# Kernel tuning notes

Measured on AMD Instinct MI355X. Metric: run time of the kernel, lower is better.

## Reference

```python
import jax, jax.numpy as jnp
import numpy as np

N_PARTS = 4
HIDDEN = 256
NUM_FREQS = 10
IN_DIM = 3
EMB_DIM = IN_DIM * (1 + 2 * NUM_FREQS)  # 63
PART_DIM = HIDDEN // N_PARTS


def _embed(x):
    freqs = 2.0 ** jnp.arange(NUM_FREQS, dtype=x.dtype)        # [F]
    xf = x[..., None, :] * freqs[:, None]                      # [..., F, 3]
    enc = jnp.stack([jnp.sin(xf), jnp.cos(xf)], axis=-2)       # [..., F, 2, 3]
    enc = enc.reshape(x.shape[:-1] + (NUM_FREQS * 2 * IN_DIM,))
    return jnp.concatenate([x, enc], axis=-1)                  # [..., 63]


def _masks():
    # contiguous 0/1 per-part neuron masks over the HIDDEN axis (ClassMaskCreator)
    m = np.zeros((N_PARTS, HIDDEN), dtype=np.float32)
    for p in range(N_PARTS):
        s = p * PART_DIM
        e = HIDDEN if p == N_PARTS - 1 else s + PART_DIM
        m[p, s:e] = 1.0
    return jnp.asarray(m)


def setup_inputs() -> dict:
    key = jax.random.key(0)
    ks = jax.random.split(key, 8)
    B, N = 1, 131072

    def lin(k, fan_in, fan_out):
        return jax.random.normal(k, (fan_in, fan_out), jnp.float32) / np.float32(np.sqrt(fan_in))

    return {
        "coords": jax.random.normal(ks[0], (B, N, IN_DIM), jnp.float32),
        "W0": lin(ks[1], EMB_DIM, HIDDEN), "b0": jnp.zeros((HIDDEN,), jnp.float32),
        "W1": lin(ks[2], HIDDEN, HIDDEN), "b1": jnp.zeros((HIDDEN,), jnp.float32),
        "W2": lin(ks[3], HIDDEN, HIDDEN), "b2": jnp.zeros((HIDDEN,), jnp.float32),
        "Wocc": lin(ks[4], HIDDEN, 1), "bocc": jnp.zeros((1,), jnp.float32),
        "Wc": jax.random.normal(ks[5], (N_PARTS, HIDDEN), jnp.float32) / np.float32(np.sqrt(HIDDEN)),
        "bc": jnp.zeros((N_PARTS,), jnp.float32),
    }


def reference(coords, W0, b0, W1, b1, W2, b2, Wocc, bocc, Wc, bc):
    masks = _masks()                                  # [P, H]
    x = _embed(coords) @ W0 + b0                      # [B, N, H]  (no activation after layer 0, per source)

    # occupancy trunk: relu(L1) -> relu(L2) -> occ head
    x_occ = jax.nn.relu(x @ W1 + b1)
    x_occ = jax.nn.relu(x_occ @ W2 + b2)
    occ = x_occ @ Wocc + bocc                         # [B, N, 1]

    # part branches. Loop iteration i=0 masks x; i=1 indexes temporal_part_output[1*part_id],
    # i.e. the i=0 outputs. The i=1 outputs (h2) are dead w.r.t. all returned values because
    # part_features[part_id] for part_id in 0..P-1 selects the first P (i=0) entries.
    h1 = [jax.nn.relu((x * masks[p]) @ W1 + b1) for p in range(N_PARTS)]  # [B, N, H] each

    # class heads: class_heads[p](h1[p] * mask_p).squeeze(0), concatenated on last dim
    cls = [jnp.squeeze((h1[p] * masks[p]) @ Wc[p][:, None] + bc[p], axis=0)
           for p in range(N_PARTS)]                   # [N, 1] each (B == 1)
    part_class = jnp.concatenate(cls, axis=-1)        # [N, P]

    return occ, part_class
```

## Files before the change

kernel.cpp:

```cpp
#include <hip/hip_runtime.h>


#define NPTS 131072
#define M_PB 128
#define AST 256

typedef _Float16 half8   __attribute__((ext_vector_type(8)));
typedef _Float16 half4_t __attribute__((ext_vector_type(4)));
typedef __fp16   fp16x2  __attribute__((ext_vector_type(2)));
typedef float    float4_t __attribute__((ext_vector_type(4)));

__global__ void prep(const float* __restrict__ W0, const float* __restrict__ W1,
                     const float* __restrict__ W2, _Float16* __restrict__ ws) {
  int id = blockIdx.x * 256 + threadIdx.x;
  _Float16 v;
  if (id < 16384) {
    int e = id, j = e & 7, l = (e >> 3) & 63, tn = (e >> 9) & 3, kb = (e >> 11) & 1, s = e >> 12;
    int k = kb * 32 + (l >> 4) * 8 + j, n = s * 64 + tn * 16 + (l & 15);
    v = (k < 63) ? (_Float16)W0[k * 256 + n] : (_Float16)0.f;
  } else if (id < 81920) {
    int e = id - 16384, j = e & 7, l = (e >> 3) & 63, tn = (e >> 9) & 3, kb = (e >> 11) & 7, s = e >> 14;
    int k = kb * 32 + (l >> 4) * 8 + j, n = s * 64 + tn * 16 + (l & 15);
    v = (_Float16)W1[k * 256 + n];
  } else {
    int e = id - 81920, j = e & 7, l = (e >> 3) & 63, tn = (e >> 9) & 3, kb = (e >> 11) & 7, s = e >> 14;
    int k = kb * 32 + (l >> 4) * 8 + j, n = s * 64 + tn * 16 + (l & 15);
    v = (_Float16)W2[k * 256 + n];
  }
  ws[id] = v;
}

__device__ __forceinline__ half4_t pack4(float a, float b, float cc, float d) {
  fp16x2 p0 = __builtin_amdgcn_cvt_pkrtz(a, b);
  fp16x2 p1 = __builtin_amdgcn_cvt_pkrtz(cc, d);
  half4_t h;
  h[0] = (_Float16)p0[0]; h[1] = (_Float16)p0[1];
  h[2] = (_Float16)p1[0]; h[3] = (_Float16)p1[1];
  return h;
}

__global__ __launch_bounds__(256, 2) void mlp_main(
    const float* __restrict__ coords,
    const _Float16* __restrict__ W0sw,
    const _Float16* __restrict__ W1sw,
    const _Float16* __restrict__ W2sw,
    const float* __restrict__ b0, const float* __restrict__ b1,
    const float* __restrict__ b2,
    const float* __restrict__ Wocc, const float* __restrict__ bocc,
    const float* __restrict__ Wc, const float* __restrict__ bc,
    float* __restrict__ out) {
  __shared__ _Float16 actX[M_PB * AST];
  __shared__ float occ_s[4][M_PB];

  const int t = threadIdx.x;
  const int w = t >> 6;
  const int l = t & 63;
  const int c = l & 15;
  const int q = l >> 4;
  const int sx = c & 7;
  const int m0 = blockIdx.x * M_PB;

  half8 a0[4], a1[4];
  {
    const _Float16* wb = W0sw + (size_t)w * 4096 + l * 8;
#pragma unroll
    for (int tn = 0; tn < 4; ++tn) {
      a0[tn] = *(const half8*)(wb + tn * 512);
      a1[tn] = *(const half8*)(wb + 2048 + tn * 512);
    }
  }

  {
    int m = t & 127, kh = (t >> 7) * 32;
    const int cb = (t >> 7) * 4;
    const int sm = m & 7;
    const float* cp = coords + (size_t)(m0 + m) * 3;
    float x0 = cp[0], x1 = cp[1], x2 = cp[2];
#pragma unroll
    for (int i = 0; i < 4; ++i) {
      float v[8];
#pragma unroll
      for (int u = 0; u < 8; ++u) {
        int k = kh + i * 8 + u;
        float r;
        if (k >= 63) r = 0.f;
        else if (k < 3) r = (k == 0) ? x0 : (k == 1 ? x1 : x2);
        else {
          int kk = k - 3;
          int f = kk / 6;
          int rem = kk - 6 * f;
          int s = (rem >= 3) ? 1 : 0;
          int i3 = rem - 3 * s;
          float xi = (i3 == 0) ? x0 : (i3 == 1 ? x1 : x2);
          float arg = xi * (float)(1 << f);
          float nn = rintf(arg * 0.15915494309189535f);
          float rr = fmaf(nn, -6.28318548202514648f, arg);
          rr = fmaf(nn, 1.7484555e-7f, rr);
          r = s ? __cosf(rr) : __sinf(rr);
        }
        v[u] = r;
      }
      half8 ev;
#pragma unroll
      for (int u = 0; u < 4; ++u) {
        fp16x2 p = __builtin_amdgcn_cvt_pkrtz(v[2 * u], v[2 * u + 1]);
        ev[2 * u] = (_Float16)p[0]; ev[2 * u + 1] = (_Float16)p[1];
      }
      *(half8*)&actX[m * AST + (((cb + i) ^ sm) << 3)] = ev;
    }
  }
  __syncthreads();

  float4_t acc[4][8];
  const _Float16* rp = actX + c * AST;

  {
#pragma unroll
    for (int tn = 0; tn < 4; ++tn) {
      float4_t bz = *(const float4_t*)(b0 + 64 * w + tn * 16 + q * 4);
#pragma unroll
      for (int tm = 0; tm < 8; ++tm) acc[tn][tm] = bz;
    }
#pragma unroll
    for (int kb = 0; kb < 2; ++kb) {
      const int cx = ((kb * 4 + q) ^ sx) << 3;
      half8 b[8];
#pragma unroll
      for (int tm = 0; tm < 8; ++tm) b[tm] = *(const half8*)(rp + tm * 16 * AST + cx);
#pragma unroll
      for (int tn = 0; tn < 4; ++tn)
#pragma unroll
        for (int tm = 0; tm < 8; ++tm)
          acc[tn][tm] = __builtin_amdgcn_mfma_f32_16x16x32_f16(
              kb ? a1[tn] : a0[tn], b[tm], acc[tn][tm], 0, 0, 0);
    }
  }
  __syncthreads();
#pragma unroll
  for (int tn = 0; tn < 4; ++tn) {
    const int sc = ((8 * w + 2 * tn + (q >> 1)) ^ sx) * 8 + (q & 1) * 4;
#pragma unroll
    for (int tm = 0; tm < 8; ++tm) {
      float4_t v = acc[tn][tm];
      *(half4_t*)&actX[(tm * 16 + c) * AST + sc] = pack4(v[0], v[1], v[2], v[3]);
    }
  }
  __syncthreads();

  {
    const _Float16* wb = W1sw + (size_t)w * 16384 + l * 8;
    const int w2 = 2 * w;
    float bcw = bc[w];
#pragma unroll
    for (int tn = 0; tn < 4; ++tn) {
      float4_t bz = *(const float4_t*)(b1 + 64 * w + tn * 16 + q * 4);
#pragma unroll
      for (int tm = 0; tm < 8; ++tm) acc[tn][tm] = bz;
    }
    auto kbof = [&](int j) {
      return (j < 2) ? (w2 + j) : ((j - 2) + ((j - 2) >= w2 ? 2 : 0));
    };
    half8 A[3][4];
#pragma unroll
    for (int p = 0; p < 3; ++p) {
      const _Float16* pa = wb + kbof(p) * 2048;
#pragma unroll
      for (int tn = 0; tn < 4; ++tn) A[p][tn] = *(const half8*)(pa + tn * 512);
    }
#pragma unroll
    for (int j = 0; j < 8; ++j) {
      const int kb = kbof(j);
      const int cx = ((kb * 4 + q) ^ sx) << 3;
      half8 b[8];
#pragma unroll
      for (int tm = 0; tm < 8; ++tm) b[tm] = *(const half8*)(rp + tm * 16 * AST + cx);
#pragma unroll
      for (int tn = 0; tn < 4; ++tn)
#pragma unroll
        for (int tm = 0; tm < 8; ++tm)
          acc[tn][tm] = __builtin_amdgcn_mfma_f32_16x16x32_f16(
              A[j % 3][tn], b[tm], acc[tn][tm], 0, 0, 0);
      if (j == 1) {
        float pcls[8] = {0.f, 0.f, 0.f, 0.f, 0.f, 0.f, 0.f, 0.f};
#pragma unroll
        for (int tn = 0; tn < 4; ++tn) {
          float4_t wcv = *(const float4_t*)(Wc + 256 * w + 64 * w + tn * 16 + q * 4);
#pragma unroll
          for (int tm = 0; tm < 8; ++tm) {
            float4_t v = acc[tn][tm];
#pragma unroll
            for (int r = 0; r < 4; ++r) pcls[tm] += fmaxf(v[r], 0.f) * wcv[r];
          }
        }
#pragma unroll
        for (int tm = 0; tm < 8; ++tm) {
          float s = pcls[tm];
          s += __shfl_xor(s, 16, 64);
          s += __shfl_xor(s, 32, 64);
          if (l < 16)
            out[(size_t)NPTS + (size_t)(m0 + tm * 16 + c) * 4 + w] = s + bcw;
        }
      }
      if (j + 3 < 8) {
        const _Float16* pa = wb + kbof(j + 3) * 2048;
#pragma unroll
        for (int tn = 0; tn < 4; ++tn) A[j % 3][tn] = *(const half8*)(pa + tn * 512);
      }
    }
  }
  __syncthreads();
#pragma unroll
  for (int tn = 0; tn < 4; ++tn) {
    const int sc = ((8 * w + 2 * tn + (q >> 1)) ^ sx) * 8 + (q & 1) * 4;
#pragma unroll
    for (int tm = 0; tm < 8; ++tm) {
      float4_t v = acc[tn][tm];
      *(half4_t*)&actX[(tm * 16 + c) * AST + sc] =
          pack4(fmaxf(v[0], 0.f), fmaxf(v[1], 0.f), fmaxf(v[2], 0.f), fmaxf(v[3], 0.f));
    }
  }
  __syncthreads();

  {
    const _Float16* wb = W2sw + (size_t)w * 16384 + l * 8;
#pragma unroll
    for (int tn = 0; tn < 4; ++tn) {
      float4_t bz = *(const float4_t*)(b2 + 64 * w + tn * 16 + q * 4);
#pragma unroll
      for (int tm = 0; tm < 8; ++tm) acc[tn][tm] = bz;
    }
    half8 A[3][4];
#pragma unroll
    for (int p = 0; p < 3; ++p)
#pragma unroll
      for (int tn = 0; tn < 4; ++tn)
        A[p][tn] = *(const half8*)(wb + p * 2048 + tn * 512);
#pragma unroll
    for (int kb = 0; kb < 8; ++kb) {
      const int cx = ((kb * 4 + q) ^ sx) << 3;
      half8 b[8];
#pragma unroll
      for (int tm = 0; tm < 8; ++tm) b[tm] = *(const half8*)(rp + tm * 16 * AST + cx);
#pragma unroll
      for (int tn = 0; tn < 4; ++tn)
#pragma unroll
        for (int tm = 0; tm < 8; ++tm)
          acc[tn][tm] = __builtin_amdgcn_mfma_f32_16x16x32_f16(
              A[kb % 3][tn], b[tm], acc[tn][tm], 0, 0, 0);
      if (kb + 3 < 8) {
#pragma unroll
        for (int tn = 0; tn < 4; ++tn)
          A[kb % 3][tn] = *(const half8*)(wb + (kb + 3) * 2048 + tn * 512);
      }
    }
    float pocc[8] = {0.f, 0.f, 0.f, 0.f, 0.f, 0.f, 0.f, 0.f};
#pragma unroll
    for (int tn = 0; tn < 4; ++tn) {
      float4_t wov = *(const float4_t*)(Wocc + 64 * w + tn * 16 + q * 4);
#pragma unroll
      for (int tm = 0; tm < 8; ++tm) {
        float4_t v = acc[tn][tm];
#pragma unroll
        for (int r = 0; r < 4; ++r) pocc[tm] += fmaxf(v[r], 0.f) * wov[r];
      }
    }
#pragma unroll
    for (int tm = 0; tm < 8; ++tm) {
      float s = pocc[tm];
      s += __shfl_xor(s, 16, 64);
      s += __shfl_xor(s, 32, 64);
      if (l < 16) occ_s[w][tm * 16 + c] = s;
    }
  }
  __syncthreads();
  if (t < M_PB) {
    out[m0 + t] = occ_s[0][t] + occ_s[1][t] + occ_s[2][t] + occ_s[3][t] + bocc[0];
  }
}

extern "C" void kernel_launch(void* const* d_in, const int* in_sizes, int n_in,
                              void* d_out, int out_size, void* d_ws, size_t ws_size,
                              hipStream_t stream) {
  const float* coords = (const float*)d_in[0];
  const float* W0   = (const float*)d_in[1];
  const float* b0   = (const float*)d_in[2];
  const float* W1   = (const float*)d_in[3];
  const float* b1   = (const float*)d_in[4];
  const float* W2   = (const float*)d_in[5];
  const float* b2   = (const float*)d_in[6];
  const float* Wocc = (const float*)d_in[7];
  const float* bocc = (const float*)d_in[8];
  const float* Wc   = (const float*)d_in[9];
  const float* bc   = (const float*)d_in[10];
  float* out = (float*)d_out;

  _Float16* ws = (_Float16*)d_ws;
  _Float16* W0sw = ws;
  _Float16* W1sw = ws + 16384;
  _Float16* W2sw = ws + 81920;

  prep<<<576, 256, 0, stream>>>(W0, W1, W2, ws);
  mlp_main<<<NPTS / M_PB, 256, 0, stream>>>(coords, W0sw, W1sw, W2sw,
                                            b0, b1, b2, Wocc, bocc, Wc, bc, out);
}
```

Before: 116.9 us.

## Switch MLP GEMMs from 16x16x32 to 32x32x16 MFMA tiles

Rewrites all three matrix stages to use 32x32x16 f16 MFMA instructions instead of 16x16x32, with a matching new swizzled weight layout in the prep kernel and new accumulator-to-LDS writeback and head-reduction indexing. Larger MFMA tiles mean fewer LDS operand loads per FLOP and fewer MFMA issues, which should cut LDS bandwidth pressure. The cost is more complex accumulator register mapping and possible changes in register pressure or LDS bank conflicts.

```diff
diff --git a/kernel.cpp b/kernel.cpp
--- a/kernel.cpp
+++ b/kernel.cpp
@@ -9,22 +9,23 @@
 typedef _Float16 half4_t __attribute__((ext_vector_type(4)));
 typedef __fp16   fp16x2  __attribute__((ext_vector_type(2)));
 typedef float    float4_t __attribute__((ext_vector_type(4)));
+typedef float    f32x16  __attribute__((ext_vector_type(16)));
 
 __global__ void prep(const float* __restrict__ W0, const float* __restrict__ W1,
                      const float* __restrict__ W2, _Float16* __restrict__ ws) {
   int id = blockIdx.x * 256 + threadIdx.x;
   _Float16 v;
   if (id < 16384) {
-    int e = id, j = e & 7, l = (e >> 3) & 63, tn = (e >> 9) & 3, kb = (e >> 11) & 1, s = e >> 12;
-    int k = kb * 32 + (l >> 4) * 8 + j, n = s * 64 + tn * 16 + (l & 15);
+    int e = id, j = e & 7, l = (e >> 3) & 63, tn = (e >> 9) & 1, ks = (e >> 10) & 3, s = e >> 12;
+    int k = ks * 16 + (l >> 5) * 8 + j, n = s * 64 + tn * 32 + (l & 31);
     v = (k < 63) ? (_Float16)W0[k * 256 + n] : (_Float16)0.f;
   } else if (id < 81920) {
-    int e = id - 16384, j = e & 7, l = (e >> 3) & 63, tn = (e >> 9) & 3, kb = (e >> 11) & 7, s = e >> 14;
-    int k = kb * 32 + (l >> 4) * 8 + j, n = s * 64 + tn * 16 + (l & 15);
+    int e = id - 16384, j = e & 7, l = (e >> 3) & 63, tn = (e >> 9) & 1, ks = (e >> 10) & 15, s = e >> 14;
+    int k = ks * 16 + (l >> 5) * 8 + j, n = s * 64 + tn * 32 + (l & 31);
     v = (_Float16)W1[k * 256 + n];
   } else {
-    int e = id - 81920, j = e & 7, l = (e >> 3) & 63, tn = (e >> 9) & 3, kb = (e >> 11) & 7, s = e >> 14;
-    int k = kb * 32 + (l >> 4) * 8 + j, n = s * 64 + tn * 16 + (l & 15);
+    int e = id - 81920, j = e & 7, l = (e >> 3) & 63, tn = (e >> 9) & 1, ks = (e >> 10) & 15, s = e >> 14;
+    int k = ks * 16 + (l >> 5) * 8 + j, n = s * 64 + tn * 32 + (l & 31);
     v = (_Float16)W2[k * 256 + n];
   }
   ws[id] = v;
@@ -37,6 +38,26 @@
   h[0] = (_Float16)p0[0]; h[1] = (_Float16)p0[1];
   h[2] = (_Float16)p1[0]; h[3] = (_Float16)p1[1];
   return h;
+}
+
+__device__ __forceinline__ float pe_val(int k, float x0, float x1, float x2) {
+  float r;
+  if (k >= 63) r = 0.f;
+  else if (k < 3) r = (k == 0) ? x0 : (k == 1 ? x1 : x2);
+  else {
+    int kk = k - 3;
+    int f = kk / 6;
+    int rem = kk - 6 * f;
+    int s = (rem >= 3) ? 1 : 0;
+    int i3 = rem - 3 * s;
+    float xi = (i3 == 0) ? x0 : (i3 == 1 ? x1 : x2);
+    float arg = xi * (float)(1 << f);
+    float nn = rintf(arg * 0.15915494309189535f);
+    float rr = fmaf(nn, -6.28318548202514648f, arg);
+    rr = fmaf(nn, 1.7484555e-7f, rr);
+    r = s ? __cosf(rr) : __sinf(rr);
+  }
+  return r;
 }
 
 __global__ __launch_bounds__(256, 2) void mlp_main(
@@ -55,20 +76,10 @@
   const int t = threadIdx.x;
   const int w = t >> 6;
   const int l = t & 63;
-  const int c = l & 15;
-  const int q = l >> 4;
-  const int sx = c & 7;
+  const int p31 = l & 31;
+  const int hi = l >> 5;
+  const int sx = l & 7;
   const int m0 = blockIdx.x * M_PB;
-
-  half8 a0[4], a1[4];
-  {
-    const _Float16* wb = W0sw + (size_t)w * 4096 + l * 8;
-#pragma unroll
-    for (int tn = 0; tn < 4; ++tn) {
-      a0[tn] = *(const half8*)(wb + tn * 512);
-      a1[tn] = *(const half8*)(wb + 2048 + tn * 512);
-    }
-  }
 
   {
     int m = t & 127, kh = (t >> 7) * 32;
@@ -80,26 +91,7 @@
     for (int i = 0; i < 4; ++i) {
       float v[8];
 #pragma unroll
-      for (int u = 0; u < 8; ++u) {
-        int k = kh + i * 8 + u;
-        float r;
-        if (k >= 63) r = 0.f;
-        else if (k < 3) r = (k == 0) ? x0 : (k == 1 ? x1 : x2);
-        else {
-          int kk = k - 3;
-          int f = kk / 6;
-          int rem = kk - 6 * f;
-          int s = (rem >= 3) ? 1 : 0;
-          int i3 = rem - 3 * s;
-          float xi = (i3 == 0) ? x0 : (i3 == 1 ? x1 : x2);
-          float arg = xi * (float)(1 << f);
-          float nn = rintf(arg * 0.15915494309189535f);
-          float rr = fmaf(nn, -6.28318548202514648f, arg);
-          rr = fmaf(nn, 1.7484555e-7f, rr);
-          r = s ? __cosf(rr) : __sinf(rr);
-        }
-        v[u] = r;
-      }
+      for (int u = 0; u < 8; ++u) v[u] = pe_val(kh + i * 8 + u, x0, x1, x2);
       half8 ev;
 #pragma unroll
       for (int u = 0; u < 4; ++u) {
@@ -111,165 +103,222 @@
   }
   __syncthreads();
 
-  float4_t acc[4][8];
-  const _Float16* rp = actX + c * AST;
+  f32x16 acc[2][4];
+  const _Float16* rp = actX + p31 * AST;
 
   {
-#pragma unroll
-    for (int tn = 0; tn < 4; ++tn) {
-      float4_t bz = *(const float4_t*)(b0 + 64 * w + tn * 16 + q * 4);
-#pragma unroll
-      for (int tm = 0; tm < 8; ++tm) acc[tn][tm] = bz;
-    }
-#pragma unroll
-    for (int kb = 0; kb < 2; ++kb) {
-      const int cx = ((kb * 4 + q) ^ sx) << 3;
-      half8 b[8];
-#pragma unroll
-      for (int tm = 0; tm < 8; ++tm) b[tm] = *(const half8*)(rp + tm * 16 * AST + cx);
-#pragma unroll
-      for (int tn = 0; tn < 4; ++tn)
-#pragma unroll
-        for (int tm = 0; tm < 8; ++tm)
-          acc[tn][tm] = __builtin_amdgcn_mfma_f32_16x16x32_f16(
-              kb ? a1[tn] : a0[tn], b[tm], acc[tn][tm], 0, 0, 0);
-    }
-  }
-  __syncthreads();
-#pragma unroll
-  for (int tn = 0; tn < 4; ++tn) {
-    const int sc = ((8 * w + 2 * tn + (q >> 1)) ^ sx) * 8 + (q & 1) * 4;
-#pragma unroll
-    for (int tm = 0; tm < 8; ++tm) {
-      float4_t v = acc[tn][tm];
-      *(half4_t*)&actX[(tm * 16 + c) * AST + sc] = pack4(v[0], v[1], v[2], v[3]);
-    }
-  }
+    const _Float16* wb = W0sw + (size_t)w * 4096 + l * 8;
+    half8 a[4][2];
+#pragma unroll
+    for (int ks = 0; ks < 4; ++ks)
+#pragma unroll
+      for (int tn = 0; tn < 2; ++tn)
+        a[ks][tn] = *(const half8*)(wb + (ks * 2 + tn) * 512);
+#pragma unroll
+    for (int tn = 0; tn < 2; ++tn) {
+      float4_t bz0 = *(const float4_t*)(b0 + 64 * w + 32 * tn + 4 * hi);
+      float4_t bz1 = *(const float4_t*)(b0 + 64 * w + 32 * tn + 8 + 4 * hi);
+      float4_t bz2 = *(const float4_t*)(b0 + 64 * w + 32 * tn + 16 + 4 * hi);
+      float4_t bz3 = *(const float4_t*)(b0 + 64 * w + 32 * tn + 24 + 4 * hi);
+#pragma unroll
+      for (int tp = 0; tp < 4; ++tp) {
+#pragma unroll
+        for (int e = 0; e < 4; ++e) {
+          acc[tn][tp][e] = bz0[e];
+          acc[tn][tp][4 + e] = bz1[e];
+          acc[tn][tp][8 + e] = bz2[e];
+          acc[tn][tp][12 + e] = bz3[e];
+        }
+      }
+    }
+#pragma unroll
+    for (int ks = 0; ks < 4; ++ks) {
+      const int cx = ((ks * 2 + hi) ^ sx) << 3;
+      half8 b[4];
+#pragma unroll
+      for (int tp = 0; tp < 4; ++tp) b[tp] = *(const half8*)(rp + tp * 32 * AST + cx);
+#pragma unroll
+      for (int tn = 0; tn < 2; ++tn)
+#pragma unroll
+        for (int tp = 0; tp < 4; ++tp)
+          acc[tn][tp] = __builtin_amdgcn_mfma_f32_32x32x16_f16(
+              a[ks][tn], b[tp], acc[tn][tp], 0, 0, 0);
+    }
+  }
+  __syncthreads();
+#pragma unroll
+  for (int tn = 0; tn < 2; ++tn)
+#pragma unroll
+    for (int bc = 0; bc < 4; ++bc) {
+      const int sc = ((8 * w + 4 * tn + bc) ^ sx) * 8 + 4 * hi;
+#pragma unroll
+      for (int tp = 0; tp < 4; ++tp) {
+        *(half4_t*)&actX[(tp * 32 + p31) * AST + sc] =
+            pack4(acc[tn][tp][4 * bc], acc[tn][tp][4 * bc + 1],
+                  acc[tn][tp][4 * bc + 2], acc[tn][tp][4 * bc + 3]);
+      }
+    }
   __syncthreads();
 
   {
     const _Float16* wb = W1sw + (size_t)w * 16384 + l * 8;
-    const int w2 = 2 * w;
+    const int w4 = 4 * w;
     float bcw = bc[w];
 #pragma unroll
-    for (int tn = 0; tn < 4; ++tn) {
-      float4_t bz = *(const float4_t*)(b1 + 64 * w + tn * 16 + q * 4);
-#pragma unroll
-      for (int tm = 0; tm < 8; ++tm) acc[tn][tm] = bz;
-    }
-    auto kbof = [&](int j) {
-      return (j < 2) ? (w2 + j) : ((j - 2) + ((j - 2) >= w2 ? 2 : 0));
+    for (int tn = 0; tn < 2; ++tn) {
+      float4_t bz0 = *(const float4_t*)(b1 + 64 * w + 32 * tn + 4 * hi);
+      float4_t bz1 = *(const float4_t*)(b1 + 64 * w + 32 * tn + 8 + 4 * hi);
+      float4_t bz2 = *(const float4_t*)(b1 + 64 * w + 32 * tn + 16 + 4 * hi);
+      float4_t bz3 = *(const float4_t*)(b1 + 64 * w + 32 * tn + 24 + 4 * hi);
+#pragma unroll
+      for (int tp = 0; tp < 4; ++tp) {
+#pragma unroll
+        for (int e = 0; e < 4; ++e) {
+          acc[tn][tp][e] = bz0[e];
+          acc[tn][tp][4 + e] = bz1[e];
+          acc[tn][tp][8 + e] = bz2[e];
+          acc[tn][tp][12 + e] = bz3[e];
+        }
+      }
+    }
+    auto ksof = [&](int j) {
+      return (j < 4) ? (w4 + j) : ((j - 4) + ((j - 4) >= w4 ? 4 : 0));
     };
-    half8 A[3][4];
+    half8 A[3][2];
 #pragma unroll
     for (int p = 0; p < 3; ++p) {
-      const _Float16* pa = wb + kbof(p) * 2048;
-#pragma unroll
-      for (int tn = 0; tn < 4; ++tn) A[p][tn] = *(const half8*)(pa + tn * 512);
-    }
-#pragma unroll
-    for (int j = 0; j < 8; ++j) {
-      const int kb = kbof(j);
-      const int cx = ((kb * 4 + q) ^ sx) << 3;
-      half8 b[8];
-#pragma unroll
-      for (int tm = 0; tm < 8; ++tm) b[tm] = *(const half8*)(rp + tm * 16 * AST + cx);
-#pragma unroll
-      for (int tn = 0; tn < 4; ++tn)
-#pragma unroll
-        for (int tm = 0; tm < 8; ++tm)
-          acc[tn][tm] = __builtin_amdgcn_mfma_f32_16x16x32_f16(
-              A[j % 3][tn], b[tm], acc[tn][tm], 0, 0, 0);
-      if (j == 1) {
-        float pcls[8] = {0.f, 0.f, 0.f, 0.f, 0.f, 0.f, 0.f, 0.f};
-#pragma unroll
-        for (int tn = 0; tn < 4; ++tn) {
-          float4_t wcv = *(const float4_t*)(Wc + 256 * w + 64 * w + tn * 16 + q * 4);
-#pragma unroll
-          for (int tm = 0; tm < 8; ++tm) {
-            float4_t v = acc[tn][tm];
-#pragma unroll
-            for (int r = 0; r < 4; ++r) pcls[tm] += fmaxf(v[r], 0.f) * wcv[r];
+      const _Float16* pa = wb + ksof(p) * 1024;
+#pragma unroll
+      for (int tn = 0; tn < 2; ++tn) A[p][tn] = *(const half8*)(pa + tn * 512);
+    }
+#pragma unroll
+    for (int j = 0; j < 16; ++j) {
+      const int ks = ksof(j);
+      const int cx = ((ks * 2 + hi) ^ sx) << 3;
+      half8 b[4];
+#pragma unroll
+      for (int tp = 0; tp < 4; ++tp) b[tp] = *(const half8*)(rp + tp * 32 * AST + cx);
+#pragma unroll
+      for (int tn = 0; tn < 2; ++tn)
+#pragma unroll
+        for (int tp = 0; tp < 4; ++tp)
+          acc[tn][tp] = __builtin_amdgcn_mfma_f32_32x32x16_f16(
+              A[j % 3][tn], b[tp], acc[tn][tp], 0, 0, 0);
+      if (j == 3) {
+        float pcls[4] = {0.f, 0.f, 0.f, 0.f};
+#pragma unroll
+        for (int tn = 0; tn < 2; ++tn) {
+          float4_t w0v = *(const float4_t*)(Wc + 256 * w + 64 * w + 32 * tn + 4 * hi);
+          float4_t w1v = *(const float4_t*)(Wc + 256 * w + 64 * w + 32 * tn + 8 + 4 * hi);
+          float4_t w2v = *(const float4_t*)(Wc + 256 * w + 64 * w + 32 * tn + 16 + 4 * hi);
+          float4_t w3v = *(const float4_t*)(Wc + 256 * w + 64 * w + 32 * tn + 24 + 4 * hi);
+#pragma unroll
+          for (int tp = 0; tp < 4; ++tp) {
+#pragma unroll
+            for (int e = 0; e < 4; ++e) {
+              pcls[tp] += fmaxf(acc[tn][tp][e], 0.f) * w0v[e];
+              pcls[tp] += fmaxf(acc[tn][tp][4 + e], 0.f) * w1v[e];
+              pcls[tp] += fmaxf(acc[tn][tp][8 + e], 0.f) * w2v[e];
+              pcls[tp] += fmaxf(acc[tn][tp][12 + e], 0.f) * w3v[e];
+            }
           }
         }
 #pragma unroll
-        for (int tm = 0; tm < 8; ++tm) {
-          float s = pcls[tm];
-          s += __shfl_xor(s, 16, 64);
+        for (int tp = 0; tp < 4; ++tp) {
+          float s = pcls[tp];
           s += __shfl_xor(s, 32, 64);
-          if (l < 16)
-            out[(size_t)NPTS + (size_t)(m0 + tm * 16 + c) * 4 + w] = s + bcw;
-        }
-      }
-      if (j + 3 < 8) {
-        const _Float16* pa = wb + kbof(j + 3) * 2048;
-#pragma unroll
-        for (int tn = 0; tn < 4; ++tn) A[j % 3][tn] = *(const half8*)(pa + tn * 512);
-      }
-    }
-  }
-  __syncthreads();
-#pragma unroll
-  for (int tn = 0; tn < 4; ++tn) {
-    const int sc = ((8 * w + 2 * tn + (q >> 1)) ^ sx) * 8 + (q & 1) * 4;
-#pragma unroll
-    for (int tm = 0; tm < 8; ++tm) {
-      float4_t v = acc[tn][tm];
-      *(half4_t*)&actX[(tm * 16 + c) * AST + sc] =
-          pack4(fmaxf(v[0], 0.f), fmaxf(v[1], 0.f), fmaxf(v[2], 0.f), fmaxf(v[3], 0.f));
-    }
-  }
+          if (l < 32)
+            out[(size_t)NPTS + (size_t)(m0 + tp * 32 + p31) * 4 + w] = s + bcw;
+        }
+      }
+      if (j + 3 < 16) {
+        const _Float16* pa = wb + ksof(j + 3) * 1024;
+#pragma unroll
+        for (int tn = 0; tn < 2; ++tn) A[j % 3][tn] = *(const half8*)(pa + tn * 512);
+      }
+    }
+  }
+  __syncthreads();
+#pragma unroll
+  for (int tn = 0; tn < 2; ++tn)
+#pragma unroll
+    for (int bc = 0; bc < 4; ++bc) {
+      const int sc = ((8 * w + 4 * tn + bc) ^ sx) * 8 + 4 * hi;
+#pragma unroll
+      for (int tp = 0; tp < 4; ++tp) {
+        *(half4_t*)&actX[(tp * 32 + p31) * AST + sc] =
+            pack4(fmaxf(acc[tn][tp][4 * bc], 0.f), fmaxf(acc[tn][tp][4 * bc + 1], 0.f),
+                  fmaxf(acc[tn][tp][4 * bc + 2], 0.f), fmaxf(acc[tn][tp][4 * bc + 3], 0.f));
+      }
+    }
   __syncthreads();
 
   {
     const _Float16* wb = W2sw + (size_t)w * 16384 + l * 8;
 #pragma unroll
-    for (int tn = 0; tn < 4; ++tn) {
-      float4_t bz = *(const float4_t*)(b2 + 64 * w + tn * 16 + q * 4);
-#pragma unroll
-      for (int tm = 0; tm < 8; ++tm) acc[tn][tm] = bz;
-    }
-    half8 A[3][4];
+    for (int tn = 0; tn < 2; ++tn) {
+      float4_t bz0 = *(const float4_t*)(b2 + 64 * w + 32 * tn + 4 * hi);
+      float4_t bz1 = *(const float4_t*)(b2 + 64 * w + 32 * tn + 8 + 4 * hi);
+      float4_t bz2 = *(const float4_t*)(b2 + 64 * w + 32 * tn + 16 + 4 * hi);
+      float4_t bz3 = *(const float4_t*)(b2 + 64 * w + 32 * tn + 24 + 4 * hi);
+#pragma unroll
+      for (int tp = 0; tp < 4; ++tp) {
+#pragma unroll
+        for (int e = 0; e < 4; ++e) {
+          acc[tn][tp][e] = bz0[e];
+          acc[tn][tp][4 + e] = bz1[e];
+          acc[tn][tp][8 + e] = bz2[e];
+          acc[tn][tp][12 + e] = bz3[e];
+        }
+      }
+    }
+    half8 A[3][2];
 #pragma unroll
     for (int p = 0; p < 3; ++p)
 #pragma unroll
-      for (int tn = 0; tn < 4; ++tn)
-        A[p][tn] = *(const half8*)(wb + p * 2048 + tn * 512);
-#pragma unroll
-    for (int kb = 0; kb < 8; ++kb) {
-      const int cx = ((kb * 4 + q) ^ sx) << 3;
-      half8 b[8];
-#pragma unroll
-      for (int tm = 0; tm < 8; ++tm) b[tm] = *(const half8*)(rp + tm * 16 * AST + cx);
-#pragma unroll
-      for (int tn = 0; tn < 4; ++tn)
-#pragma unroll
-        for (int tm = 0; tm < 8; ++tm)
-          acc[tn][tm] = __builtin_amdgcn_mfma_f32_16x16x32_f16(
-              A[kb % 3][tn], b[tm], acc[tn][tm], 0, 0, 0);
-      if (kb + 3 < 8) {
-#pragma unroll
-        for (int tn = 0; tn < 4; ++tn)
-          A[kb % 3][tn] = *(const half8*)(wb + (kb + 3) * 2048 + tn * 512);
-      }
-    }
-    float pocc[8] = {0.f, 0.f, 0.f, 0.f, 0.f, 0.f, 0.f, 0.f};
-#pragma unroll
-    for (int tn = 0; tn < 4; ++tn) {
-      float4_t wov = *(const float4_t*)(Wocc + 64 * w + tn * 16 + q * 4);
-#pragma unroll
-      for (int tm = 0; tm < 8; ++tm) {
-        float4_t v = acc[tn][tm];
-#pragma unroll
-        for (int r = 0; r < 4; ++r) pocc[tm] += fmaxf(v[r], 0.f) * wov[r];
-      }
-    }
-#pragma unroll
-    for (int tm = 0; tm < 8; ++tm) {
-      float s = pocc[tm];
-      s += __shfl_xor(s, 16, 64);
+      for (int tn = 0; tn < 2; ++tn)
+        A[p][tn] = *(const half8*)(wb + p * 1024 + tn * 512);
+#pragma unroll
+    for (int ks = 0; ks < 16; ++ks) {
+      const int cx = ((ks * 2 + hi) ^ sx) << 3;
+      half8 b[4];
+#pragma unroll
+      for (int tp = 0; tp < 4; ++tp) b[tp] = *(const half8*)(rp + tp * 32 * AST + cx);
+#pragma unroll
+      for (int tn = 0; tn < 2; ++tn)
+#pragma unroll
+        for (int tp = 0; tp < 4; ++tp)
+          acc[tn][tp] = __builtin_amdgcn_mfma_f32_32x32x16_f16(
+              A[ks % 3][tn], b[tp], acc[tn][tp], 0, 0, 0);
+      if (ks + 3 < 16) {
+#pragma unroll
+        for (int tn = 0; tn < 2; ++tn)
+          A[ks % 3][tn] = *(const half8*)(wb + (ks + 3) * 1024 + tn * 512);
+      }
+    }
+    float pocc[4] = {0.f, 0.f, 0.f, 0.f};
+#pragma unroll
+    for (int tn = 0; tn < 2; ++tn) {
+      float4_t w0v = *(const float4_t*)(Wocc + 64 * w + 32 * tn + 4 * hi);
+      float4_t w1v = *(const float4_t*)(Wocc + 64 * w + 32 * tn + 8 + 4 * hi);
+      float4_t w2v = *(const float4_t*)(Wocc + 64 * w + 32 * tn + 16 + 4 * hi);
+      float4_t w3v = *(const float4_t*)(Wocc + 64 * w + 32 * tn + 24 + 4 * hi);
+#pragma unroll
+      for (int tp = 0; tp < 4; ++tp) {
+#pragma unroll
+        for (int e = 0; e < 4; ++e) {
+          pocc[tp] += fmaxf(acc[tn][tp][e], 0.f) * w0v[e];
+          pocc[tp] += fmaxf(acc[tn][tp][4 + e], 0.f) * w1v[e];
+          pocc[tp] += fmaxf(acc[tn][tp][8 + e], 0.f) * w2v[e];
+          pocc[tp] += fmaxf(acc[tn][tp][12 + e], 0.f) * w3v[e];
+        }
+      }
+    }
+#pragma unroll
+    for (int tp = 0; tp < 4; ++tp) {
+      float s = pocc[tp];
       s += __shfl_xor(s, 32, 64);
-      if (l < 16) occ_s[w][tm * 16 + c] = s;
+      if (l < 32) occ_s[w][tp * 32 + p31] = s;
     }
   }
   __syncthreads();
```

New measurement: 117.0 us. No clear change (+0.1%).
